# Kernel tuning notes

Measured on AMD Instinct MI355X. Metric: run time of the kernel, lower is better.

Reference implementation:

```python
import jax, jax.numpy as jnp
import numpy as np

B, S, DIM = 8, 1024, 192
D2 = 2 * DIM            # inner width 384
CH = 4                  # cell heads (= qk_size)
HD = D2 // CH           # 96 head dim
NB = D2 // 4            # 96 block-diagonal blocks
BLK = D2 // NB          # block size 4
TAU = float(HD) ** 0.5


def setup_inputs() -> dict:
    key = jax.random.key(0)
    ks = jax.random.split(key, 16)
    r = lambda i, shp, s=0.02: jax.random.normal(ks[i], shp, jnp.float32) * s
    return {
        "x": jax.random.normal(ks[0], (B, S, DIM), jnp.float32),
        "ln_g": jnp.ones((DIM,), jnp.float32), "ln_b": jnp.zeros((DIM,), jnp.float32),
        "w1": r(1, (D2, DIM)), "b1": jnp.zeros((D2,), jnp.float32),
        "w2": r(2, (D2, DIM)), "b2": jnp.zeros((D2,), jnp.float32),
        "conv_w": r(3, (D2, 1, 3), 0.1), "conv_b": jnp.zeros((D2,), jnp.float32),
        "qw": r(4, (NB, BLK, BLK), 0.1), "qb": jnp.zeros((D2,), jnp.float32),
        "kw": r(5, (NB, BLK, BLK), 0.1), "kb": jnp.zeros((D2,), jnp.float32),
        "vw": r(6, (NB, BLK, BLK), 0.1), "vb": jnp.zeros((D2,), jnp.float32),
        "wi": r(7, (CH, 3 * D2)), "bi": jax.random.normal(ks[8], (CH,), jnp.float32) * 0.1,
        "wf": r(9, (CH, 3 * D2)), "bf": jnp.linspace(3.0, 6.0, CH).astype(jnp.float32),
        "gn_g": jnp.ones((D2,), jnp.float32), "gn_b": jnp.zeros((D2,), jnp.float32),
        "wo": r(10, (DIM, D2)), "bo": jnp.zeros((DIM,), jnp.float32),
        "skip": jnp.ones((D2,), jnp.float32),
    }


def _layernorm(x, g, b):
    m = x.mean(-1, keepdims=True)
    v = ((x - m) ** 2).mean(-1, keepdims=True)
    return (x - m) / jnp.sqrt(v + 1e-5) * g + b


def _blockdiag(x, w, b):
    # x: [B,S,D2] -> blocks [B,S,NB,BLK]; w: [NB, out_blk, in_blk]
    bs, sq, _ = x.shape
    y = jnp.einsum('bsni,noi->bsno', x.reshape(bs, sq, NB, BLK), w)
    return y.reshape(bs, sq, D2) + b


def _dwconv(x, w, b):
    # depthwise conv over sequence: x [B,S,C] -> [B,C,S] conv -> [B,S,C]
    y = jax.lax.conv_general_dilated(
        x.transpose(0, 2, 1), w, window_strides=(1,), padding=[(1, 1)],
        dimension_numbers=('NCH', 'OIH', 'NCH'), feature_group_count=D2)
    return y.transpose(0, 2, 1) + b


def _cell(q, k, v, wi, bi, wf, bf, gn_g, gn_b):
    bs, sq, _ = q.shape
    gi = jnp.concatenate([q, k, v], axis=-1)                      # [B,S,3*D2]
    it = jnp.einsum('bsc,hc->bhs', gi, wi) + bi[None, :, None]    # [B,H,S]
    ft = jnp.einsum('bsc,hc->bhs', gi, wf) + bf[None, :, None]
    c = jnp.cumsum(jax.nn.log_sigmoid(ft), axis=-1)               # [B,H,S]
    logm = c[..., :, None] - c[..., None, :]                      # cum[i]-cum[j]
    mask = jnp.tril(jnp.ones((sq, sq), dtype=bool))
    f_act = jnp.where(mask, logm, -jnp.inf)
    dt = f_act + it[:, :, None, :]                                # add itilde over cols
    max_d = jnp.max(dt, axis=-1, keepdims=True)
    dmat = jnp.exp(dt - max_d)                                    # [B,H,S,S]
    qh = q.reshape(bs, sq, CH, HD).transpose(0, 2, 1, 3)
    kh = k.reshape(bs, sq, CH, HD).transpose(0, 2, 1, 3)
    vh = v.reshape(bs, sq, CH, HD).transpose(0, 2, 1, 3)
    ct = jnp.einsum('bhid,bhjd->bhij', qh, kh) * dmat / TAU
    maxit = jnp.maximum(jnp.abs(ct.sum(-1, keepdims=True)), jnp.exp(-max_d))
    h = jnp.einsum('bhij,bhjd->bhid', ct, vh) / (maxit + 1e-6)
    h = h.transpose(0, 2, 1, 3).reshape(bs, sq, CH, HD)           # per-token GroupNorm
    mu = h.mean(-1, keepdims=True)
    var = ((h - mu) ** 2).mean(-1, keepdims=True)
    h = (h - mu) / jnp.sqrt(var + 1e-5)
    h = h * gn_g.reshape(CH, HD) + gn_b.reshape(CH, HD)
    return h.reshape(bs, sq, D2)


def reference(x, ln_g, ln_b, w1, b1, w2, b2, conv_w, conv_b, qw, qb, kw, kb,
              vw, vb, wi, bi, wf, bf, gn_g, gn_b, wo, bo, skip):
    inputs = _layernorm(x, ln_g, ln_b)
    a = inputs @ w1.T + b1                   # [B,S,D2]
    bgate = jax.nn.silu(inputs @ w2.T + b2)  # [B,S,D2]
    qk = jax.nn.silu(_dwconv(a, conv_w, conv_b))
    q = _blockdiag(qk, qw, qb)
    k = _blockdiag(qk, kw, kb)
    v = _blockdiag(a, vw, vb)
    out1 = _cell(q, k, v, wi, bi, wf, bf, gn_g, gn_b)
    out1 = (out1 + skip * qk) * bgate
    out = out1 @ wo.T + bo
    return out + x
```

## Files before the change

### kernel.cpp

```cpp
#include <hip/hip_runtime.h>
#include <cstdint>

#define TAU_ 9.797958971132712f

typedef __attribute__((ext_vector_type(4))) float f32x4;
typedef __attribute__((ext_vector_type(8))) short short8;

#define DEV static __device__ __forceinline__

DEV unsigned short f2bf(float f){
  union { float f; unsigned u; } v; v.f = f;
  unsigned r = v.u + 0x7FFFu + ((v.u >> 16) & 1u);
  return (unsigned short)(r >> 16);
}
DEV float bf2f(unsigned short u){
  union { unsigned u; float f; } v; v.u = ((unsigned)u) << 16; return v.f;
}
DEV unsigned pack2bf(float a, float b){
  unsigned r;
  asm("v_cvt_pk_bf16_f32 %0, %1, %2" : "=v"(r) : "v"(a), "v"(b));
  return r;
}
DEV f32x4 ld_bf4(const unsigned short* p){
  uint2 r = *(const uint2*)p;
  f32x4 o;
  o[0] = bf2f((unsigned short)(r.x & 0xffff));
  o[1] = bf2f((unsigned short)(r.x >> 16));
  o[2] = bf2f((unsigned short)(r.y & 0xffff));
  o[3] = bf2f((unsigned short)(r.y >> 16));
  return o;
}
DEV float siluf_(float x){ return x / (1.f + __expf(-x)); }
DEV float logsigf_(float x){ return fminf(x, 0.f) - log1pf(__expf(-fabsf(x))); }

__global__ __launch_bounds__(256) void k1a_ln(
    const float* __restrict__ x, const float* __restrict__ ln_g, const float* __restrict__ ln_b,
    short* __restrict__ xnbf)
{
  const int tid = threadIdx.x;
  const int t = blockIdx.x * 16 + (tid >> 4);
  const int g = tid & 15;
  const float* xr = x + (long)t * 192 + g * 12;
  f32x4 v0 = *(const f32x4*)(xr);
  f32x4 v1 = *(const f32x4*)(xr + 4);
  f32x4 v2 = *(const f32x4*)(xr + 8);
  float s  = v0[0]+v0[1]+v0[2]+v0[3] + v1[0]+v1[1]+v1[2]+v1[3] + v2[0]+v2[1]+v2[2]+v2[3];
  float sq = v0[0]*v0[0]+v0[1]*v0[1]+v0[2]*v0[2]+v0[3]*v0[3]
           + v1[0]*v1[0]+v1[1]*v1[1]+v1[2]*v1[2]+v1[3]*v1[3]
           + v2[0]*v2[0]+v2[1]*v2[1]+v2[2]*v2[2]+v2[3]*v2[3];
  s  += __shfl_xor(s, 1);  s  += __shfl_xor(s, 2);  s  += __shfl_xor(s, 4);  s  += __shfl_xor(s, 8);
  sq += __shfl_xor(sq, 1); sq += __shfl_xor(sq, 2); sq += __shfl_xor(sq, 4); sq += __shfl_xor(sq, 8);
  const float mean = s * (1.f/192.f);
  const float rstd = rsqrtf(sq * (1.f/192.f) - mean * mean + 1e-5f);
  const int c0 = g * 12;
  f32x4 g0 = *(const f32x4*)(ln_g + c0),     b0 = *(const f32x4*)(ln_b + c0);
  f32x4 g1 = *(const f32x4*)(ln_g + c0 + 4), b1 = *(const f32x4*)(ln_b + c0 + 4);
  f32x4 g2 = *(const f32x4*)(ln_g + c0 + 8), b2 = *(const f32x4*)(ln_b + c0 + 8);
  unsigned pk[6];
  pk[0] = pack2bf((v0[0]-mean)*rstd*g0[0]+b0[0], (v0[1]-mean)*rstd*g0[1]+b0[1]);
  pk[1] = pack2bf((v0[2]-mean)*rstd*g0[2]+b0[2], (v0[3]-mean)*rstd*g0[3]+b0[3]);
  pk[2] = pack2bf((v1[0]-mean)*rstd*g1[0]+b1[0], (v1[1]-mean)*rstd*g1[1]+b1[1]);
  pk[3] = pack2bf((v1[2]-mean)*rstd*g1[2]+b1[2], (v1[3]-mean)*rstd*g1[3]+b1[3]);
  pk[4] = pack2bf((v2[0]-mean)*rstd*g2[0]+b2[0], (v2[1]-mean)*rstd*g2[1]+b2[1]);
  pk[5] = pack2bf((v2[2]-mean)*rstd*g2[2]+b2[2], (v2[3]-mean)*rstd*g2[3]+b2[3]);
  uint2* xo = (uint2*)(xnbf + (long)t * 192 + g * 12);
  xo[0] = make_uint2(pk[0], pk[1]);
  xo[1] = make_uint2(pk[2], pk[3]);
  xo[2] = make_uint2(pk[4], pk[5]);
}

__global__ __launch_bounds__(256) void k1b_gemm(
    const short* __restrict__ xnbf,
    const float* __restrict__ w1, const float* __restrict__ w2,
    const float* __restrict__ b1, const float* __restrict__ b2,
    unsigned short* __restrict__ abf, unsigned short* __restrict__ bgate)
{
  __shared__ short wt[18432];
  const int tid = threadIdx.x;
  const int ntg = blockIdx.x & 7;
  const int t0 = (blockIdx.x >> 3) * 64;
  {
    const float* src = (ntg < 4 ? w1 : w2) + (long)(ntg & 3) * 96 * 192;
    #pragma unroll
    for(int i = 0; i < 9; i++){
      const int u = i * 256 + tid;
      const int row = u / 24;
      const int dst = (u * 16) ^ ((row & 7) << 4);
      f32x4 f0 = *(const f32x4*)(src + u * 8);
      f32x4 f1 = *(const f32x4*)(src + u * 8 + 4);
      uint4 pk;
      pk.x = pack2bf(f0[0], f0[1]); pk.y = pack2bf(f0[2], f0[3]);
      pk.z = pack2bf(f1[0], f1[1]); pk.w = pack2bf(f1[2], f1[3]);
      *(uint4*)((char*)wt + dst) = pk;
    }
  }
  __syncthreads();
  const int widx = tid >> 6, lane = tid & 63, qg = lane >> 4, l16 = lane & 15;
  const int mrow = widx * 16 + l16;
  f32x4 acc[6];
  #pragma unroll
  for(int nt = 0; nt < 6; nt++) acc[nt] = (f32x4){0.f,0.f,0.f,0.f};
  const short* xrow = xnbf + (long)(t0 + mrow) * 192;
  #pragma unroll
  for(int kc = 0; kc < 6; kc++){
    short8 af = *(const short8*)(xrow + kc * 32 + 8 * qg);
    #pragma unroll
    for(int nt = 0; nt < 6; nt++){
      const int row = nt * 16 + l16;
      int byte = row * 384 + (kc * 32 + 8 * qg) * 2;
      byte ^= (row & 7) << 4;
      short8 bfr = *(const short8*)((const char*)wt + byte);
      acc[nt] = __builtin_amdgcn_mfma_f32_16x16x32_bf16(af, bfr, acc[nt], 0, 0, 0);
    }
  }
  const int half = ntg >> 2;
  const float* bias = half ? b2 : b1;
  const int ncol = (ntg & 3) * 96;
  #pragma unroll
  for(int nt = 0; nt < 6; nt++){
    const int n = ncol + nt * 16 + l16;
    const float bs = bias[n];
    #pragma unroll
    for(int r = 0; r < 4; r++){
      const int trow = t0 + widx * 16 + 4 * qg + r;
      float v = acc[nt][r] + bs;
      if(half) bgate[(long)trow * 384 + n] = f2bf(siluf_(v));
      else     abf[(long)trow * 384 + n] = f2bf(v);
    }
  }
}

__global__ __launch_bounds__(256) void k2bv(
    const unsigned short* __restrict__ abf,
    const float* __restrict__ cw, const float* __restrict__ cb,
    const float* __restrict__ qw, const float* __restrict__ qb,
    const float* __restrict__ kw, const float* __restrict__ kb,
    const float* __restrict__ vw, const float* __restrict__ vb,
    unsigned short* __restrict__ qkbf, short* __restrict__ qbf, short* __restrict__ kbf,
    short* __restrict__ vbf, short* __restrict__ vtbf)
{
  __shared__ float vt[64][97];
  const int tid = threadIdx.x;
  const int bh = blockIdx.x >> 4;
  const int b = bh >> 2, h = bh & 3;
  const int s0 = (blockIdx.x & 15) << 6;
  #pragma unroll
  for(int it = 0; it < 6; it++){
    const int f = it * 256 + tid;
    const int sl = f / 24, c4l = f % 24;
    const int c4 = h * 24 + c4l;
    const int s = s0 + sl;
    const long t = (long)b * 1024 + s;
    const long abase = t * 384 + c4 * 4;
    f32x4 am = ld_bf4(abf + abase);
    f32x4 al = (s > 0)    ? ld_bf4(abf + abase - 384) : (f32x4){0.f,0.f,0.f,0.f};
    f32x4 ar = (s < 1023) ? ld_bf4(abf + abase + 384) : (f32x4){0.f,0.f,0.f,0.f};
    f32x4 cw0 = *(const f32x4*)(cw + c4 * 12);
    f32x4 cw1 = *(const f32x4*)(cw + c4 * 12 + 4);
    f32x4 cw2 = *(const f32x4*)(cw + c4 * 12 + 8);
    f32x4 cb4 = *(const f32x4*)(cb + c4 * 4);
    f32x4 in;
    in[0] = siluf_(cb4[0] + al[0]*cw0[0] + am[0]*cw0[1] + ar[0]*cw0[2]);
    in[1] = siluf_(cb4[1] + al[1]*cw0[3] + am[1]*cw1[0] + ar[1]*cw1[1]);
    in[2] = siluf_(cb4[2] + al[2]*cw1[2] + am[2]*cw1[3] + ar[2]*cw2[0]);
    in[3] = siluf_(cb4[3] + al[3]*cw2[1] + am[3]*cw2[2] + ar[3]*cw2[3]);
    {
      uint2 pk; pk.x = pack2bf(in[0], in[1]); pk.y = pack2bf(in[2], in[3]);
      *(uint2*)(qkbf + abase) = pk;
    }
    const long base = ((long)(b * 4 + h) * 1024 + s) * 96 + c4l * 4;
    {
      const float* w = qw + c4 * 16;
      float v0 = qb[c4*4+0] + w[0]*in[0]  + w[1]*in[1]  + w[2]*in[2]  + w[3]*in[3];
      float v1 = qb[c4*4+1] + w[4]*in[0]  + w[5]*in[1]  + w[6]*in[2]  + w[7]*in[3];
      float v2 = qb[c4*4+2] + w[8]*in[0]  + w[9]*in[1]  + w[10]*in[2] + w[11]*in[3];
      float v3 = qb[c4*4+3] + w[12]*in[0] + w[13]*in[1] + w[14]*in[2] + w[15]*in[3];
      uint2 pk; pk.x = pack2bf(v0, v1); pk.y = pack2bf(v2, v3);
      *(uint2*)(qbf + base) = pk;
    }
    {
      const float* w = kw + c4 * 16;
      float v0 = kb[c4*4+0] + w[0]*in[0]  + w[1]*in[1]  + w[2]*in[2]  + w[3]*in[3];
      float v1 = kb[c4*4+1] + w[4]*in[0]  + w[5]*in[1]  + w[6]*in[2]  + w[7]*in[3];
      float v2 = kb[c4*4+2] + w[8]*in[0]  + w[9]*in[1]  + w[10]*in[2] + w[11]*in[3];
      float v3 = kb[c4*4+3] + w[12]*in[0] + w[13]*in[1] + w[14]*in[2] + w[15]*in[3];
      uint2 pk; pk.x = pack2bf(v0, v1); pk.y = pack2bf(v2, v3);
      *(uint2*)(kbf + base) = pk;
    }
    {
      const float* w = vw + c4 * 16;
      float vv[4];
      #pragma unroll
      for(int o = 0; o < 4; o++){
        float v = vb[c4*4+o] + w[o*4]*am[0] + w[o*4+1]*am[1] + w[o*4+2]*am[2] + w[o*4+3]*am[3];
        vv[o] = v;
        vt[sl][c4l * 4 + o] = v;
      }
      uint2 pk; pk.x = pack2bf(vv[0], vv[1]); pk.y = pack2bf(vv[2], vv[3]);
      *(uint2*)(vbf + abase) = pk;
    }
  }
  __syncthreads();
  #pragma unroll
  for(int it = 0; it < 24; it++){
    const int f = it * 256 + tid;
    const int d = f >> 6, sl = f & 63;
    vtbf[((long)bh * 96 + d) * 1024 + s0 + sl] = (short)f2bf(vt[sl][d]);
  }
}

__global__ __launch_bounds__(256) void k2c_gates(
    const short* __restrict__ qbf, const short* __restrict__ kbf, const short* __restrict__ vbf,
    const float* __restrict__ wi, const float* __restrict__ bi,
    const float* __restrict__ wf, const float* __restrict__ bff,
    float* __restrict__ itv, float* __restrict__ ftv)
{
  __shared__ short wg[8 * 1160];
  const int tid = threadIdx.x;
  const int t0 = blockIdx.x * 64;
  #pragma unroll
  for(int i = 0; i < 9; i++){
    const int u = i * 256 + tid;
    const int row = u / 288, col4 = u % 288;
    const float* src = ((row < 4) ? wi + row * 1152 : wf + (row - 4) * 1152) + col4 * 4;
    f32x4 v = *(const f32x4*)src;
    uint2 pk; pk.x = pack2bf(v[0], v[1]); pk.y = pack2bf(v[2], v[3]);
    *(uint2*)(&wg[row * 1160 + col4 * 4]) = pk;
  }
  __syncthreads();
  const int w = tid >> 6, lane = tid & 63, qg = lane >> 4, l16 = lane & 15;
  const int tw = t0 + w * 16;
  const int tA = tw + l16;
  const int b = tA >> 10, s = tA & 1023;
  f32x4 acc = (f32x4){0.f,0.f,0.f,0.f};
  #pragma unroll
  for(int kc = 0; kc < 36; kc++){
    const int blk = kc / 3;
    const int off = (kc % 3) * 32 + qg * 8;
    short8 af;
    if(blk < 4)      af = *(const short8*)(qbf + ((long)(b*4+blk)*1024 + s)*96 + off);
    else if(blk < 8) af = *(const short8*)(kbf + ((long)(b*4+blk-4)*1024 + s)*96 + off);
    else             af = *(const short8*)(vbf + (long)tA*384 + (blk-8)*96 + off);
    short8 bf8 = *(const short8*)(&wg[(l16 & 7) * 1160 + kc * 32 + qg * 8]);
    acc = __builtin_amdgcn_mfma_f32_16x16x32_bf16(af, bf8, acc, 0, 0, 0);
  }
  if(l16 < 8){
    const int gh = l16 & 3;
    const float bias = (l16 < 4) ? bi[gh] : bff[gh];
    float* dst = (l16 < 4) ? itv : ftv;
    #pragma unroll
    for(int r = 0; r < 4; r++){
      const int t = tw + 4 * qg + r;
      dst[((long)((t >> 10) * 4 + gh)) * 1024 + (t & 1023)] = acc[r] + bias;
    }
  }
}

__global__ __launch_bounds__(256) void k3_scan(
    const float* __restrict__ itv, const float* __restrict__ ftv,
    float* __restrict__ Ev, float* __restrict__ Rpv, float* __restrict__ dsv)
{
  __shared__ float sb[256];
  const int bh = blockIdx.x, tid = threadIdx.x;
  const long base = (long)bh * 1024 + tid * 4;
  f32x4 f4 = *(const f32x4*)(ftv + base);
  const float l0 = logsigf_(f4[0]);
  const float l1 = logsigf_(f4[1]);
  const float l2 = logsigf_(f4[2]);
  const float l3 = logsigf_(f4[3]);
  float c0 = l0, c1 = l0 + l1, c2 = c1 + l2, c3 = c2 + l3;
  sb[tid] = c3;
  __syncthreads();
  for(int off = 1; off < 256; off <<= 1){
    float mine = sb[tid];
    float oth = (tid >= off) ? sb[tid - off] : 0.f;
    __syncthreads();
    sb[tid] = mine + oth;
    __syncthreads();
  }
  const float excl = (tid > 0) ? sb[tid - 1] : 0.f;
  c0 += excl; c1 += excl; c2 += excl; c3 += excl;
  f32x4 i4 = *(const f32x4*)(itv + base);
  const float m0 = i4[0] - c0, m1 = i4[1] - c1, m2 = i4[2] - c2, m3 = i4[3] - c3;
  const float x1 = fmaxf(m0, m1), x2 = fmaxf(x1, m2), x3 = fmaxf(x2, m3);
  __syncthreads();
  sb[tid] = x3;
  __syncthreads();
  for(int off = 1; off < 256; off <<= 1){
    float mine = sb[tid];
    float oth = (tid >= off) ? sb[tid - off] : -3.4e38f;
    __syncthreads();
    sb[tid] = fmaxf(mine, oth);
    __syncthreads();
  }
  const float exm = (tid > 0) ? sb[tid - 1] : -3.4e38f;
  const float M0 = fmaxf(m0, exm);
  const float M1 = fmaxf(x1, exm);
  const float M2 = fmaxf(x2, exm);
  const float M3 = fmaxf(x3, exm);
  f32x4 e, rp, ds;
  e[0] = __expf(m0); e[1] = __expf(m1); e[2] = __expf(m2); e[3] = __expf(m3);
  rp[0] = __expf(-M0) * (1.f/TAU_); rp[1] = __expf(-M1) * (1.f/TAU_);
  rp[2] = __expf(-M2) * (1.f/TAU_); rp[3] = __expf(-M3) * (1.f/TAU_);
  ds[0] = __expf(-(c0 + M0)); ds[1] = __expf(-(c1 + M1));
  ds[2] = __expf(-(c2 + M2)); ds[3] = __expf(-(c3 + M3));
  *(f32x4*)(Ev  + base) = e;
  *(f32x4*)(Rpv + base) = rp;
  *(f32x4*)(dsv + base) = ds;
}

__global__ __launch_bounds__(256, 2) void k4_attn(
    const short* __restrict__ qbf, const short* __restrict__ kbf, const short* __restrict__ vtbf,
    const float* __restrict__ Ev, const float* __restrict__ Rpv, const float* __restrict__ dsv,
    const float* __restrict__ gn_g, const float* __restrict__ gn_b,
    const unsigned short* __restrict__ qkbf, const unsigned short* __restrict__ bgate,
    const float* __restrict__ skip, short* __restrict__ o1bf)
{
  __shared__ short kbuf[2][64 * 104];
  __shared__ short vbuf[2][96 * 72];
  __shared__ float ebuf[2][64];
  __shared__ short P[4][16][72];
  const int tid = threadIdx.x;
  const int w = tid >> 6, lane = tid & 63, qg = lane >> 4, l16 = lane & 15;
  const int xcd = blockIdx.x & 7, q = blockIdx.x >> 3;
  const int bh = ((q & 3) << 3) | xcd;
  const int qh = q >> 2;
  const int ib = (q < 32) ? (15 - qh) : (qh - 8);
  const int i0w = ib * 64 + w * 16;
  const long qkbase = (long)bh * 1024;
  const int nj = ib + 1;

  short8 qf[3];
  #pragma unroll
  for(int kc = 0; kc < 3; kc++)
    qf[kc] = *(const short8*)(qbf + (qkbase + i0w + l16) * 96 + kc * 32 + 8 * qg);
  const float rp = Rpv[qkbase + i0w + l16];
  const float ds = dsv[qkbase + i0w + l16];

  f32x4 acc[6];
  #pragma unroll
  for(int dt = 0; dt < 6; dt++) acc[dt] = (f32x4){0.f,0.f,0.f,0.f};
  float bp = 0.f;

  const int rK0 = tid / 12,        cK0 = tid % 12;
  const int rK1 = (tid+256) / 12,  cK1 = (tid+256) % 12;
  const int rK2 = (tid+512) / 12,  cK2 = (tid+512) % 12;
  const int dV0 = tid >> 3,        cV0 = tid & 7;
  const int dV1 = (tid+256) >> 3,  cV1 = (tid+256) & 7;
  const int dV2 = (tid+512) >> 3,  cV2 = (tid+512) & 7;
  const bool he = (tid < 16);
  short8 sk0, sk1, sk2, sv0, sv1, sv2; f32x4 se;
  const short* kgb = kbf + qkbase * 96;
  const short* vgb = vtbf + (long)bh * 96 * 1024;

#define STAGE_LOAD(J0)                                              \
  {                                                                 \
    const int j0_ = (J0);                                           \
    sk0 = *(const short8*)(kgb + (j0_ + rK0) * 96 + cK0 * 8);       \
    sk1 = *(const short8*)(kgb + (j0_ + rK1) * 96 + cK1 * 8);       \
    sk2 = *(const short8*)(kgb + (j0_ + rK2) * 96 + cK2 * 8);       \
    sv0 = *(const short8*)(vgb + (long)dV0 * 1024 + j0_ + cV0 * 8); \
    sv1 = *(const short8*)(vgb + (long)dV1 * 1024 + j0_ + cV1 * 8); \
    sv2 = *(const short8*)(vgb + (long)dV2 * 1024 + j0_ + cV2 * 8); \
    if(he) se = *(const f32x4*)(Ev + qkbase + j0_ + tid * 4);       \
  }

#define STAGE_WRITE(B)                                   \
  {                                                      \
    *(short8*)(&kbuf[B][rK0 * 104 + cK0 * 8]) = sk0;     \
    *(short8*)(&kbuf[B][rK1 * 104 + cK1 * 8]) = sk1;     \
    *(short8*)(&kbuf[B][rK2 * 104 + cK2 * 8]) = sk2;     \
    *(short8*)(&vbuf[B][dV0 * 72 + cV0 * 8]) = sv0;      \
    *(short8*)(&vbuf[B][dV1 * 72 + cV1 * 8]) = sv1;      \
    *(short8*)(&vbuf[B][dV2 * 72 + cV2 * 8]) = sv2;      \
    if(he) *(f32x4*)(&ebuf[B][tid * 4]) = se;            \
  }

  STAGE_LOAD(0);
  int cur = 0;
  for(int jt = 0; jt < nj; jt++){
    STAGE_WRITE(cur);
    __syncthreads();
    if(jt + 1 < nj) STAGE_LOAD((jt + 1) * 64);

    const int j0 = jt * 64;
    const bool diag = (jt == nj - 1);
    const int i = i0w + l16;
    __builtin_amdgcn_s_setprio(1);
    #pragma unroll
    for(int jsub = 0; jsub < 4; jsub++){
      f32x4 C = (f32x4){0.f,0.f,0.f,0.f};
      #pragma unroll
      for(int kc = 0; kc < 3; kc++){
        short8 kf = *(const short8*)(&kbuf[cur][(jsub*16 + l16) * 104 + kc * 32 + 8 * qg]);
        C = __builtin_amdgcn_mfma_f32_16x16x32_bf16(kf, qf[kc], C, 0, 0, 0);
      }
      f32x4 e4 = *(const f32x4*)(&ebuf[cur][jsub * 16 + 4 * qg]);
      float v0 = C[0] * e4[0];
      float v1 = C[1] * e4[1];
      float v2 = C[2] * e4[2];
      float v3 = C[3] * e4[3];
      if(diag){
        const int jb = j0 + jsub * 16 + 4 * qg;
        if(jb + 0 > i) v0 = 0.f;
        if(jb + 1 > i) v1 = 0.f;
        if(jb + 2 > i) v2 = 0.f;
        if(jb + 3 > i) v3 = 0.f;
      }
      bp += v0 + v1 + v2 + v3;
      uint2 pw; pw.x = pack2bf(v0, v1); pw.y = pack2bf(v2, v3);
      *(uint2*)(&P[w][l16][jsub * 16 + 4 * qg]) = pw;
    }
    asm volatile("s_waitcnt lgkmcnt(0)" ::: "memory");
    #pragma unroll
    for(int ksub = 0; ksub < 2; ksub++){
      short8 pa = *(const short8*)(&P[w][l16][ksub * 32 + 8 * qg]);
      #pragma unroll
      for(int dt = 0; dt < 6; dt++){
        short8 vf = *(const short8*)(&vbuf[cur][(dt * 16 + l16) * 72 + ksub * 32 + 8 * qg]);
        acc[dt] = __builtin_amdgcn_mfma_f32_16x16x32_bf16(pa, vf, acc[dt], 0, 0, 0);
      }
    }
    __builtin_amdgcn_s_setprio(0);
    cur ^= 1;
  }
#undef STAGE_LOAD
#undef STAGE_WRITE

  const int head = bh & 3, bb = bh >> 2;
  float bsum = bp;
  bsum += __shfl_xor(bsum, 16);
  bsum += __shfl_xor(bsum, 32);
  const float bfull = bsum * rp;
  const float den = fmaxf(fabsf(bfull), ds) + 1e-6f;
  const float sc = rp / den;
  float srow[4];
  #pragma unroll
  for(int r = 0; r < 4; r++) srow[r] = __shfl(sc, 4 * qg + r);
  float hv[6][4], mu[4], rs[4];
  #pragma unroll
  for(int r = 0; r < 4; r++){
    float sm = 0.f, sq = 0.f;
    #pragma unroll
    for(int dt = 0; dt < 6; dt++){
      const float h = acc[dt][r] * srow[r];
      hv[dt][r] = h; sm += h; sq += h * h;
    }
    sm += __shfl_xor(sm, 1); sm += __shfl_xor(sm, 2); sm += __shfl_xor(sm, 4); sm += __shfl_xor(sm, 8);
    sq += __shfl_xor(sq, 1); sq += __shfl_xor(sq, 2); sq += __shfl_xor(sq, 4); sq += __shfl_xor(sq, 8);
    const float m_ = sm * (1.f/96.f);
    mu[r] = m_;
    rs[r] = rsqrtf(sq * (1.f/96.f) - m_ * m_ + 1e-5f);
  }
  __syncthreads();
  short* hstage = &kbuf[0][0];
  #pragma unroll
  for(int dt = 0; dt < 6; dt++){
    const int col = head * 96 + dt * 16 + l16;
    const float g  = gn_g[col];
    const float be = gn_b[col];
    #pragma unroll
    for(int r = 0; r < 4; r++){
      const float hn = (hv[dt][r] - mu[r]) * rs[r] * g + be;
      hstage[(w * 16 + 4 * qg + r) * 104 + dt * 16 + l16] = (short)f2bf(hn);
    }
  }
  __syncthreads();
  #pragma unroll
  for(int u2 = 0; u2 < 3; u2++){
    const int f = u2 * 256 + tid;
    const int row = f / 12, c8 = f % 12;
    const long off = ((long)(bb * 1024 + ib * 64 + row)) * 384 + head * 96 + c8 * 8;
    short8 h8 = *(const short8*)(hstage + row * 104 + c8 * 8);
    short8 q8 = *(const short8*)((const short*)qkbf + off);
    short8 g8 = *(const short8*)((const short*)bgate + off);
    f32x4 s0 = *(const f32x4*)(skip + head * 96 + c8 * 8);
    f32x4 s1 = *(const f32x4*)(skip + head * 96 + c8 * 8 + 4);
    float o[8];
    #pragma unroll
    for(int i = 0; i < 8; i++){
      const float sk = (i < 4) ? s0[i] : s1[i - 4];
      o[i] = (bf2f((unsigned short)h8[i]) + sk * bf2f((unsigned short)q8[i]))
             * bf2f((unsigned short)g8[i]);
    }
    union { short8 s; unsigned u4[4]; } ov;
    ov.u4[0] = pack2bf(o[0], o[1]); ov.u4[1] = pack2bf(o[2], o[3]);
    ov.u4[2] = pack2bf(o[4], o[5]); ov.u4[3] = pack2bf(o[6], o[7]);
    *(short8*)(o1bf + off) = ov.s;
  }
}

__global__ __launch_bounds__(256) void k5_gemm(
    const short* __restrict__ o1bf, const float* __restrict__ wo,
    const float* __restrict__ bo, const float* __restrict__ x, float* __restrict__ out)
{
  __shared__ short wt[18432];
  const int tid = threadIdx.x;
  const int ng = blockIdx.x & 3;
  const int t0 = (blockIdx.x >> 2) * 64;
  {
    const float* src = wo + (long)ng * 48 * 384;
    #pragma unroll
    for(int i = 0; i < 9; i++){
      const int u = i * 256 + tid;
      const int row = u / 48;
      const int dst = (u * 16) ^ ((row & 7) << 4);
      f32x4 f0 = *(const f32x4*)(src + u * 8);
      f32x4 f1 = *(const f32x4*)(src + u * 8 + 4);
      uint4 pk;
      pk.x = pack2bf(f0[0], f0[1]); pk.y = pack2bf(f0[2], f0[3]);
      pk.z = pack2bf(f1[0], f1[1]); pk.w = pack2bf(f1[2], f1[3]);
      *(uint4*)((char*)wt + dst) = pk;
    }
  }
  __syncthreads();
  const int widx = tid >> 6, lane = tid & 63, qg = lane >> 4, l16 = lane & 15;
  f32x4 acc[3];
  #pragma unroll
  for(int nt = 0; nt < 3; nt++) acc[nt] = (f32x4){0.f,0.f,0.f,0.f};
  const short* arow = o1bf + (long)(t0 + widx * 16 + l16) * 384;
  #pragma unroll
  for(int kc = 0; kc < 12; kc++){
    short8 af = *(const short8*)(arow + kc * 32 + 8 * qg);
    #pragma unroll
    for(int nt = 0; nt < 3; nt++){
      const int row = nt * 16 + l16;
      int byte = row * 768 + kc * 64 + qg * 16;
      byte ^= (row & 7) << 4;
      short8 bfr = *(const short8*)((const char*)wt + byte);
      acc[nt] = __builtin_amdgcn_mfma_f32_16x16x32_bf16(af, bfr, acc[nt], 0, 0, 0);
    }
  }
  #pragma unroll
  for(int nt = 0; nt < 3; nt++){
    const int n = ng * 48 + nt * 16 + l16;
    const float b_ = bo[n];
    #pragma unroll
    for(int r = 0; r < 4; r++){
      const int trow = t0 + widx * 16 + 4 * qg + r;
      out[(long)trow * 192 + n] = acc[nt][r] + b_ + x[(long)trow * 192 + n];
    }
  }
}

extern "C" void kernel_launch(void* const* d_in, const int* in_sizes, int n_in,
                              void* d_out, int out_size, void* d_ws, size_t ws_size,
                              hipStream_t stream)
{
  (void)in_sizes; (void)n_in; (void)out_size; (void)ws_size;
  const float* x    = (const float*)d_in[0];
  const float* ln_g = (const float*)d_in[1];
  const float* ln_b = (const float*)d_in[2];
  const float* w1   = (const float*)d_in[3];
  const float* b1   = (const float*)d_in[4];
  const float* w2   = (const float*)d_in[5];
  const float* b2   = (const float*)d_in[6];
  const float* cw   = (const float*)d_in[7];
  const float* cb   = (const float*)d_in[8];
  const float* qw   = (const float*)d_in[9];
  const float* qb   = (const float*)d_in[10];
  const float* kw   = (const float*)d_in[11];
  const float* kb   = (const float*)d_in[12];
  const float* vw   = (const float*)d_in[13];
  const float* vb   = (const float*)d_in[14];
  const float* wi   = (const float*)d_in[15];
  const float* bi   = (const float*)d_in[16];
  const float* wf   = (const float*)d_in[17];
  const float* bff  = (const float*)d_in[18];
  const float* gn_g = (const float*)d_in[19];
  const float* gn_b = (const float*)d_in[20];
  const float* wo   = (const float*)d_in[21];
  const float* bo   = (const float*)d_in[22];
  const float* skip = (const float*)d_in[23];
  float* out = (float*)d_out;

  char* ws = (char*)d_ws;
  unsigned short* abf   = (unsigned short*)(ws + 0);
  short* vbf   = (short*)(ws + 6291456);
  unsigned short* bgate = (unsigned short*)(ws + 12582912);
  unsigned short* qkbf  = (unsigned short*)(ws + 25165824);
  short* xnbf  = (short*)(ws + 37748736);
  short* o1bf  = (short*)(ws + 41943040);
  short* qbf   = (short*)(ws + 50331648);
  short* kbf   = (short*)(ws + 56623104);
  short* vtbf  = (short*)(ws + 62914560);
  float* itv   = (float*)(ws + 69648384);
  float* ftv   = (float*)(ws + 69779456);
  float* Ev    = (float*)(ws + 69910528);
  float* Rpv   = (float*)(ws + 70041600);
  float* dsv   = (float*)(ws + 70172672);

  k1a_ln<<<512, 256, 0, stream>>>(x, ln_g, ln_b, xnbf);
  k1b_gemm<<<1024, 256, 0, stream>>>(xnbf, w1, w2, b1, b2, abf, bgate);
  k2bv<<<512, 256, 0, stream>>>(abf, cw, cb, qw, qb, kw, kb, vw, vb, qkbf, qbf, kbf, vbf, vtbf);
  k2c_gates<<<128, 256, 0, stream>>>(qbf, kbf, vbf, wi, bi, wf, bff, itv, ftv);
  k3_scan<<<32, 256, 0, stream>>>(itv, ftv, Ev, Rpv, dsv);
  k4_attn<<<512, 256, 0, stream>>>(qbf, kbf, vtbf, Ev, Rpv, dsv, gn_g, gn_b,
                                   qkbf, bgate, skip, o1bf);
  k5_gemm<<<512, 256, 0, stream>>>(o1bf, wo, bo, x, out);
}
```

Before: 78.85 us.

## Pre-convert GEMM weights to bf16 once and double M-tile per block

Extra blocks in the layernorm kernel convert w1, w2 and wo from fp32 to bf16 into workspace once per call. The two GEMM kernels then copy bf16 weights straight into LDS instead of each block re-converting fp32. Each wave also computes two 16-row M tiles, so blocks cover 128 tokens and half as many blocks are launched. This is meant to cut redundant weight loads and conversions and reuse each LDS B-fragment twice, at the cost of more accumulator registers and fewer blocks.

```diff
diff --git a/kernel.cpp b/kernel.cpp
--- a/kernel.cpp
+++ b/kernel.cpp
@@ -35,9 +35,21 @@
 
 __global__ __launch_bounds__(256) void k1a_ln(
     const float* __restrict__ x, const float* __restrict__ ln_g, const float* __restrict__ ln_b,
-    short* __restrict__ xnbf)
+    const float* __restrict__ w1, const float* __restrict__ w2, const float* __restrict__ wo,
+    short* __restrict__ xnbf, short* __restrict__ w12bf, short* __restrict__ wobf)
 {
   const int tid = threadIdx.x;
+  if(blockIdx.x >= 512){
+    const int idx4 = (blockIdx.x - 512) * 256 + tid;
+    const float* src; short* dst; int off;
+    if(idx4 < 18432)      { src = w1; dst = w12bf;         off = idx4; }
+    else if(idx4 < 36864) { src = w2; dst = w12bf + 73728; off = idx4 - 18432; }
+    else                  { src = wo; dst = wobf;          off = idx4 - 36864; }
+    f32x4 v = *(const f32x4*)(src + off * 4);
+    uint2 pk; pk.x = pack2bf(v[0], v[1]); pk.y = pack2bf(v[2], v[3]);
+    *(uint2*)(dst + off * 4) = pk;
+    return;
+  }
   const int t = blockIdx.x * 16 + (tid >> 4);
   const int g = tid & 15;
   const float* xr = x + (long)t * 192 + g * 12;
@@ -70,62 +82,64 @@
 }
 
 __global__ __launch_bounds__(256) void k1b_gemm(
-    const short* __restrict__ xnbf,
-    const float* __restrict__ w1, const float* __restrict__ w2,
+    const short* __restrict__ xnbf, const short* __restrict__ w12bf,
     const float* __restrict__ b1, const float* __restrict__ b2,
     unsigned short* __restrict__ abf, unsigned short* __restrict__ bgate)
 {
   __shared__ short wt[18432];
   const int tid = threadIdx.x;
   const int ntg = blockIdx.x & 7;
-  const int t0 = (blockIdx.x >> 3) * 64;
+  const int t0 = (blockIdx.x >> 3) * 128;
   {
-    const float* src = (ntg < 4 ? w1 : w2) + (long)(ntg & 3) * 96 * 192;
+    const short* src = w12bf + (long)ntg * 96 * 192;
     #pragma unroll
     for(int i = 0; i < 9; i++){
       const int u = i * 256 + tid;
       const int row = u / 24;
       const int dst = (u * 16) ^ ((row & 7) << 4);
-      f32x4 f0 = *(const f32x4*)(src + u * 8);
-      f32x4 f1 = *(const f32x4*)(src + u * 8 + 4);
-      uint4 pk;
-      pk.x = pack2bf(f0[0], f0[1]); pk.y = pack2bf(f0[2], f0[3]);
-      pk.z = pack2bf(f1[0], f1[1]); pk.w = pack2bf(f1[2], f1[3]);
-      *(uint4*)((char*)wt + dst) = pk;
+      *(short8*)((char*)wt + dst) = *(const short8*)(src + u * 8);
     }
   }
   __syncthreads();
   const int widx = tid >> 6, lane = tid & 63, qg = lane >> 4, l16 = lane & 15;
-  const int mrow = widx * 16 + l16;
-  f32x4 acc[6];
-  #pragma unroll
-  for(int nt = 0; nt < 6; nt++) acc[nt] = (f32x4){0.f,0.f,0.f,0.f};
-  const short* xrow = xnbf + (long)(t0 + mrow) * 192;
+  const int m0 = t0 + widx * 32;
+  f32x4 acc[2][6];
+  #pragma unroll
+  for(int mt = 0; mt < 2; mt++)
+    #pragma unroll
+    for(int nt = 0; nt < 6; nt++) acc[mt][nt] = (f32x4){0.f,0.f,0.f,0.f};
+  const short* xrow0 = xnbf + (long)(m0 + l16) * 192;
+  const short* xrow1 = xnbf + (long)(m0 + 16 + l16) * 192;
   #pragma unroll
   for(int kc = 0; kc < 6; kc++){
-    short8 af = *(const short8*)(xrow + kc * 32 + 8 * qg);
+    short8 af0 = *(const short8*)(xrow0 + kc * 32 + 8 * qg);
+    short8 af1 = *(const short8*)(xrow1 + kc * 32 + 8 * qg);
     #pragma unroll
     for(int nt = 0; nt < 6; nt++){
       const int row = nt * 16 + l16;
       int byte = row * 384 + (kc * 32 + 8 * qg) * 2;
       byte ^= (row & 7) << 4;
       short8 bfr = *(const short8*)((const char*)wt + byte);
-      acc[nt] = __builtin_amdgcn_mfma_f32_16x16x32_bf16(af, bfr, acc[nt], 0, 0, 0);
+      acc[0][nt] = __builtin_amdgcn_mfma_f32_16x16x32_bf16(af0, bfr, acc[0][nt], 0, 0, 0);
+      acc[1][nt] = __builtin_amdgcn_mfma_f32_16x16x32_bf16(af1, bfr, acc[1][nt], 0, 0, 0);
     }
   }
   const int half = ntg >> 2;
   const float* bias = half ? b2 : b1;
   const int ncol = (ntg & 3) * 96;
   #pragma unroll
-  for(int nt = 0; nt < 6; nt++){
-    const int n = ncol + nt * 16 + l16;
-    const float bs = bias[n];
-    #pragma unroll
-    for(int r = 0; r < 4; r++){
-      const int trow = t0 + widx * 16 + 4 * qg + r;
-      float v = acc[nt][r] + bs;
-      if(half) bgate[(long)trow * 384 + n] = f2bf(siluf_(v));
-      else     abf[(long)trow * 384 + n] = f2bf(v);
+  for(int mt = 0; mt < 2; mt++){
+    #pragma unroll
+    for(int nt = 0; nt < 6; nt++){
+      const int n = ncol + nt * 16 + l16;
+      const float bs = bias[n];
+      #pragma unroll
+      for(int r = 0; r < 4; r++){
+        const int trow = m0 + mt * 16 + 4 * qg + r;
+        float v = acc[mt][nt][r] + bs;
+        if(half) bgate[(long)trow * 384 + n] = f2bf(siluf_(v));
+        else     abf[(long)trow * 384 + n] = f2bf(v);
+      }
     }
   }
 }
@@ -491,54 +505,58 @@
 }
 
 __global__ __launch_bounds__(256) void k5_gemm(
-    const short* __restrict__ o1bf, const float* __restrict__ wo,
+    const short* __restrict__ o1bf, const short* __restrict__ wobf,
     const float* __restrict__ bo, const float* __restrict__ x, float* __restrict__ out)
 {
   __shared__ short wt[18432];
   const int tid = threadIdx.x;
   const int ng = blockIdx.x & 3;
-  const int t0 = (blockIdx.x >> 2) * 64;
+  const int t0 = (blockIdx.x >> 2) * 128;
   {
-    const float* src = wo + (long)ng * 48 * 384;
+    const short* src = wobf + (long)ng * 48 * 384;
     #pragma unroll
     for(int i = 0; i < 9; i++){
       const int u = i * 256 + tid;
       const int row = u / 48;
       const int dst = (u * 16) ^ ((row & 7) << 4);
-      f32x4 f0 = *(const f32x4*)(src + u * 8);
-      f32x4 f1 = *(const f32x4*)(src + u * 8 + 4);
-      uint4 pk;
-      pk.x = pack2bf(f0[0], f0[1]); pk.y = pack2bf(f0[2], f0[3]);
-      pk.z = pack2bf(f1[0], f1[1]); pk.w = pack2bf(f1[2], f1[3]);
-      *(uint4*)((char*)wt + dst) = pk;
+      *(short8*)((char*)wt + dst) = *(const short8*)(src + u * 8);
     }
   }
   __syncthreads();
   const int widx = tid >> 6, lane = tid & 63, qg = lane >> 4, l16 = lane & 15;
-  f32x4 acc[3];
-  #pragma unroll
-  for(int nt = 0; nt < 3; nt++) acc[nt] = (f32x4){0.f,0.f,0.f,0.f};
-  const short* arow = o1bf + (long)(t0 + widx * 16 + l16) * 384;
+  const int m0 = t0 + widx * 32;
+  f32x4 acc[2][3];
+  #pragma unroll
+  for(int mt = 0; mt < 2; mt++)
+    #pragma unroll
+    for(int nt = 0; nt < 3; nt++) acc[mt][nt] = (f32x4){0.f,0.f,0.f,0.f};
+  const short* arow0 = o1bf + (long)(m0 + l16) * 384;
+  const short* arow1 = o1bf + (long)(m0 + 16 + l16) * 384;
   #pragma unroll
   for(int kc = 0; kc < 12; kc++){
-    short8 af = *(const short8*)(arow + kc * 32 + 8 * qg);
+    short8 af0 = *(const short8*)(arow0 + kc * 32 + 8 * qg);
+    short8 af1 = *(const short8*)(arow1 + kc * 32 + 8 * qg);
     #pragma unroll
     for(int nt = 0; nt < 3; nt++){
       const int row = nt * 16 + l16;
       int byte = row * 768 + kc * 64 + qg * 16;
       byte ^= (row & 7) << 4;
       short8 bfr = *(const short8*)((const char*)wt + byte);
-      acc[nt] = __builtin_amdgcn_mfma_f32_16x16x32_bf16(af, bfr, acc[nt], 0, 0, 0);
-    }
-  }
-  #pragma unroll
-  for(int nt = 0; nt < 3; nt++){
-    const int n = ng * 48 + nt * 16 + l16;
-    const float b_ = bo[n];
-    #pragma unroll
-    for(int r = 0; r < 4; r++){
-      const int trow = t0 + widx * 16 + 4 * qg + r;
-      out[(long)trow * 192 + n] = acc[nt][r] + b_ + x[(long)trow * 192 + n];
+      acc[0][nt] = __builtin_amdgcn_mfma_f32_16x16x32_bf16(af0, bfr, acc[0][nt], 0, 0, 0);
+      acc[1][nt] = __builtin_amdgcn_mfma_f32_16x16x32_bf16(af1, bfr, acc[1][nt], 0, 0, 0);
+    }
+  }
+  #pragma unroll
+  for(int mt = 0; mt < 2; mt++){
+    #pragma unroll
+    for(int nt = 0; nt < 3; nt++){
+      const int n = ng * 48 + nt * 16 + l16;
+      const float b_ = bo[n];
+      #pragma unroll
+      for(int r = 0; r < 4; r++){
+        const int trow = m0 + mt * 16 + 4 * qg + r;
+        out[(long)trow * 192 + n] = acc[mt][nt][r] + b_ + x[(long)trow * 192 + n];
+      }
     }
   }
 }
@@ -580,6 +598,8 @@
   unsigned short* bgate = (unsigned short*)(ws + 12582912);
   unsigned short* qkbf  = (unsigned short*)(ws + 25165824);
   short* xnbf  = (short*)(ws + 37748736);
+  short* w12bf = (short*)(ws + 40894464);
+  short* wobf  = (short*)(ws + 41189376);
   short* o1bf  = (short*)(ws + 41943040);
   short* qbf   = (short*)(ws + 50331648);
   short* kbf   = (short*)(ws + 56623104);
@@ -590,12 +610,12 @@
   float* Rpv   = (float*)(ws + 70041600);
   float* dsv   = (float*)(ws + 70172672);
 
-  k1a_ln<<<512, 256, 0, stream>>>(x, ln_g, ln_b, xnbf);
-  k1b_gemm<<<1024, 256, 0, stream>>>(xnbf, w1, w2, b1, b2, abf, bgate);
+  k1a_ln<<<728, 256, 0, stream>>>(x, ln_g, ln_b, w1, w2, wo, xnbf, w12bf, wobf);
+  k1b_gemm<<<512, 256, 0, stream>>>(xnbf, w12bf, b1, b2, abf, bgate);
   k2bv<<<512, 256, 0, stream>>>(abf, cw, cb, qw, qb, kw, kb, vw, vb, qkbf, qbf, kbf, vbf, vtbf);
   k2c_gates<<<128, 256, 0, stream>>>(qbf, kbf, vbf, wi, bi, wf, bff, itv, ftv);
   k3_scan<<<32, 256, 0, stream>>>(itv, ftv, Ev, Rpv, dsv);
   k4_attn<<<512, 256, 0, stream>>>(qbf, kbf, vtbf, Ev, Rpv, dsv, gn_g, gn_b,
                                    qkbf, bgate, skip, o1bf);
-  k5_gemm<<<512, 256, 0, stream>>>(o1bf, wo, bo, x, out);
-}
+  k5_gemm<<<256, 256, 0, stream>>>(o1bf, wobf, bo, x, out);
+}
```

Result: no change. 78.77 us (-0.1%).
